# Kernel optimization log

Hardware: AMD Instinct MI355X
Metric: run time of the kernel (lower is better)

The kernel has to match this reference:

```python
import jax, jax.numpy as jnp
import numpy as np

D_MODEL = 1024
N_HEADS = 16
HEAD_DIM = D_MODEL // N_HEADS  # 64


def setup_inputs() -> dict:
    key = jax.random.key(0)
    k1, k2, k3 = jax.random.split(key, 3)
    x = jax.random.normal(k1, (2, 2048, D_MODEL), dtype=jnp.float32)
    # nn.Linear(d, 3d, bias=False): store transposed so y = x @ W
    w_qkv = jax.random.normal(k2, (D_MODEL, 3 * D_MODEL), dtype=jnp.float32) * (D_MODEL ** -0.5)
    w_proj = jax.random.normal(k3, (D_MODEL, D_MODEL), dtype=jnp.float32) * (D_MODEL ** -0.5)
    return {"x": x, "w_qkv": w_qkv, "w_proj": w_proj}


def reference(x, w_qkv, w_proj):
    b, n, _ = x.shape
    qkv = x @ w_qkv  # [b, n, 3*d_model]
    # einops 'b n (h d qkv) -> qkv b h n d': qkv axis is innermost of the split
    qkv = qkv.reshape(b, n, N_HEADS, HEAD_DIM, 3)
    q = jnp.moveaxis(qkv[..., 0], 1, 2)  # [b, h, n, d]
    k = jnp.moveaxis(qkv[..., 1], 1, 2)
    v = jnp.moveaxis(qkv[..., 2], 1, 2)
    scale = HEAD_DIM ** -0.5
    scores = jnp.einsum('bhqd,bhkd->bhqk', q, k) * scale  # [b, h, n, n]
    causal = jnp.tril(jnp.ones((n, n), dtype=bool))
    scores = jnp.where(causal[None, None], scores, -jnp.inf)
    attn = jax.nn.softmax(scores, axis=-1)
    out = jnp.einsum('bhqk,bhkd->bhqd', attn, v)  # [b, h, n, d]
    out = jnp.moveaxis(out, 1, 2).reshape(b, n, D_MODEL)  # 'b h n d -> b n (h d)'
    return out @ w_proj
```

## Files before the change

### kernel.cpp

```cpp
#include <hip/hip_runtime.h>
#include <cstdint>
#include <cstddef>

#define D_MODEL 1024
#define N_HEADS 16
#define HEAD_DIM 64
#define SEQ 2048
#define BATCH 2

typedef __attribute__((ext_vector_type(8))) short bf16x8;
typedef __attribute__((ext_vector_type(4))) float f32x4;

__device__ inline unsigned short f2bf(float f) {
    union { float f; unsigned u; } v; v.f = f;
    unsigned r = v.u + 0x7fffu + ((v.u >> 16) & 1u);
    return (unsigned short)(r >> 16);
}

__device__ __forceinline__ void gload_lds16(const unsigned short* g, unsigned short* l) {
    __builtin_amdgcn_global_load_lds(
        (const __attribute__((address_space(1))) unsigned int*)g,
        (__attribute__((address_space(3))) unsigned int*)l, 16, 0, 0);
}

__global__ __launch_bounds__(256) void convert_x_kernel(
    const float* __restrict__ X, unsigned short* __restrict__ Xb)
{
    const int idx = blockIdx.x * 256 + threadIdx.x;
    const float4* src = (const float4*)X;
    float4 v0 = src[idx * 2], v1 = src[idx * 2 + 1];
    union { unsigned short u[8]; uint4 v; } o;
    o.u[0] = f2bf(v0.x); o.u[1] = f2bf(v0.y); o.u[2] = f2bf(v0.z); o.u[3] = f2bf(v0.w);
    o.u[4] = f2bf(v1.x); o.u[5] = f2bf(v1.y); o.u[6] = f2bf(v1.z); o.u[7] = f2bf(v1.w);
    ((uint4*)Xb)[idx] = o.v;
}

__global__ __launch_bounds__(256) void convert_transpose_kernel(
    const float* __restrict__ W, unsigned short* __restrict__ Wt,
    int ncols, int nrows)
{
    __shared__ float t[32][33];
    const int c0 = blockIdx.x * 32, r0 = blockIdx.y * 32;
    const int a = threadIdx.x & 31, b = threadIdx.x >> 5;
#pragma unroll
    for (int i = 0; i < 32; i += 8)
        t[b + i][a] = W[(size_t)(r0 + b + i) * ncols + c0 + a];
    __syncthreads();
#pragma unroll
    for (int i = 0; i < 32; i += 8)
        Wt[(size_t)(c0 + b + i) * nrows + r0 + a] = f2bf(t[a][b + i]);
}

#define GEMM_MFMA_BODY(A_, B_, Kdim)                                           \
    const int tid = threadIdx.x;                                               \
    const int w = tid >> 6, lane = tid & 63;                                   \
    const int l15 = lane & 15, quad = lane >> 4;                               \
    const int wr = w >> 1, wc = w & 1;                                         \
    const int row0 = blockIdx.y * 128, col0 = blockIdx.x * 128;                \
    __shared__ unsigned short As[8192];                                        \
    __shared__ unsigned short Bs[8192];                                        \
    const f32x4 zero4 = {0.f, 0.f, 0.f, 0.f};                                  \
    f32x4 acc[4][4];                                                           \
    _Pragma("unroll") for (int i = 0; i < 4; i++)                              \
        _Pragma("unroll") for (int j = 0; j < 4; j++) acc[i][j] = zero4;       \
    for (int k0 = 0; k0 < (Kdim); k0 += 64) {                                  \
        __syncthreads();                                                       \
        _Pragma("unroll") for (int f = 0; f < 4; f++) {                        \
            const int fa = w * 4 + f;                                          \
            const int mt = fa >> 1, kt = fa & 1;                               \
            const int kcol = k0 + kt * 32 + quad * 8;                          \
            gload_lds16((A_) + (size_t)(row0 + mt * 16 + l15) * (Kdim) + kcol, \
                        &As[fa * 512 + lane * 8]);                             \
            gload_lds16((B_) + (size_t)(col0 + mt * 16 + l15) * (Kdim) + kcol, \
                        &Bs[fa * 512 + lane * 8]);                             \
        }                                                                      \
        __syncthreads();                                                       \
        _Pragma("unroll") for (int kt = 0; kt < 2; kt++) {                     \
            bf16x8 af[4], bf[4];                                               \
            _Pragma("unroll") for (int i = 0; i < 4; i++)                      \
                af[i] = *(const bf16x8*)&As[((wr * 4 + i) * 2 + kt) * 512 + lane * 8]; \
            _Pragma("unroll") for (int j = 0; j < 4; j++)                      \
                bf[j] = *(const bf16x8*)&Bs[((wc * 4 + j) * 2 + kt) * 512 + lane * 8]; \
            _Pragma("unroll") for (int i = 0; i < 4; i++)                      \
                _Pragma("unroll") for (int j = 0; j < 4; j++)                  \
                    acc[i][j] = __builtin_amdgcn_mfma_f32_16x16x32_bf16(       \
                        af[i], bf[j], acc[i][j], 0, 0, 0);                     \
        }                                                                      \
    }

__global__ __launch_bounds__(256) void gemm_qkv_mfma(
    const unsigned short* __restrict__ A, const unsigned short* __restrict__ B,
    unsigned short* __restrict__ Q, unsigned short* __restrict__ Kq,
    unsigned short* __restrict__ Vt)
{
    GEMM_MFMA_BODY(A, B, D_MODEL)
#pragma unroll
    for (int i = 0; i < 4; i++) {
#pragma unroll
        for (int r = 0; r < 4; r++) {
            const int row = row0 + wr * 64 + i * 16 + quad * 4 + r;
            const int bb = row >> 11, n = row & (SEQ - 1);
#pragma unroll
            for (int j = 0; j < 4; j++) {
                const int c = col0 + wc * 64 + j * 16 + l15;
                const int which = c % 3;
                const int dd = (c / 3) & (HEAD_DIM - 1);
                const int h = c / (3 * HEAD_DIM);
                const int bh = bb * N_HEADS + h;
                const unsigned short v = f2bf(acc[i][j][r]);
                if (which == 0)
                    Q[((size_t)bh * SEQ + n) * HEAD_DIM + dd] = v;
                else if (which == 1)
                    Kq[((size_t)bh * SEQ + n) * HEAD_DIM + dd] = v;
                else
                    Vt[((size_t)bh * HEAD_DIM + dd) * SEQ + n] = v;
            }
        }
    }
}

__global__ __launch_bounds__(256) void gemm_proj_mfma(
    const unsigned short* __restrict__ A, const unsigned short* __restrict__ B,
    float* __restrict__ C)
{
    GEMM_MFMA_BODY(A, B, D_MODEL)
#pragma unroll
    for (int i = 0; i < 4; i++) {
#pragma unroll
        for (int r = 0; r < 4; r++) {
            const int row = row0 + wr * 64 + i * 16 + quad * 4 + r;
#pragma unroll
            for (int j = 0; j < 4; j++) {
                const int c = col0 + wc * 64 + j * 16 + l15;
                C[(size_t)row * D_MODEL + c] = acc[i][j][r];
            }
        }
    }
}

#define PSTR 72

__global__ __launch_bounds__(256) void flash_attn_kernel(
    const unsigned short* __restrict__ Q,
    const unsigned short* __restrict__ K,
    const unsigned short* __restrict__ Vt,
    unsigned short* __restrict__ O)
{
    const int idx = blockIdx.x;
    const int bh = idx & 31;
    const int qt2 = idx >> 5;
    const int hi = qt2 >> 3, lo = qt2 & 7;
    const int qt = (hi == 0) ? lo : (hi == 1) ? 31 - lo : (hi == 2) ? lo + 8 : 23 - lo;

    const int tid = threadIdx.x;
    const int w = tid >> 6, lane = tid & 63;
    const int l15 = lane & 15, quad = lane >> 4;

    __shared__ unsigned short Ks[2][4096];
    __shared__ unsigned short Vs[2][4096];
    __shared__ unsigned short Ps[4][16 * PSTR];

    bf16x8 qf[2];
    {
        const unsigned short* qrow =
            Q + ((size_t)bh * SEQ + qt * 64 + w * 16 + l15) * HEAD_DIM;
        qf[0] = *(const bf16x8*)(qrow + quad * 8);
        qf[1] = *(const bf16x8*)(qrow + 32 + quad * 8);
    }

    const f32x4 zero4 = {0.f, 0.f, 0.f, 0.f};
    f32x4 o_acc[4] = {zero4, zero4, zero4, zero4};
    float m_i = -1e30f, l_i = 0.f;

    auto stage = [&](int bf, int kt_t) {
        const int key0 = kt_t * 64;
#pragma unroll
        for (int i = 0; i < 2; i++) {
            const int f = w * 2 + i;
            const int ct = f >> 1, kh = f & 1;
            gload_lds16(K + ((size_t)bh * SEQ + key0 + ct * 16 + l15) * HEAD_DIM
                          + kh * 32 + quad * 8,
                        &Ks[bf][f * 512 + lane * 8]);
            gload_lds16(Vt + ((size_t)bh * HEAD_DIM + ct * 16 + l15) * SEQ
                           + key0 + kh * 32 + quad * 8,
                        &Vs[bf][f * 512 + lane * 8]);
        }
    };

    stage(0, 0);
    int buf = 0;

    const int qg = qt * 64 + w * 16 + l15;

    for (int kt = 0; kt <= qt; kt++) {
        __syncthreads();
        if (kt < qt) stage(buf ^ 1, kt + 1);

        f32x4 st[4] = {zero4, zero4, zero4, zero4};
#pragma unroll
        for (int kh = 0; kh < 2; kh++) {
#pragma unroll
            for (int ct = 0; ct < 4; ct++) {
                bf16x8 kf = *(const bf16x8*)&Ks[buf][(ct * 2 + kh) * 512 + lane * 8];
                st[ct] = __builtin_amdgcn_mfma_f32_16x16x32_bf16(kf, qf[kh], st[ct], 0, 0, 0);
            }
        }

        const bool diag = (kt == qt);
        float mt = -1e30f;
#pragma unroll
        for (int ct = 0; ct < 4; ct++) {
#pragma unroll
            for (int r = 0; r < 4; r++) {
                float v = st[ct][r] * 0.125f;
                const int kg = kt * 64 + ct * 16 + quad * 4 + r;
                if (diag && kg > qg) v = -1e30f;
                st[ct][r] = v;
                mt = fmaxf(mt, v);
            }
        }
        mt = fmaxf(mt, __shfl_xor(mt, 16));
        mt = fmaxf(mt, __shfl_xor(mt, 32));

        const float mn = fmaxf(m_i, mt);
        const float alpha = __expf(m_i - mn);
        m_i = mn;

        float ls = 0.f;
#pragma unroll
        for (int ct = 0; ct < 4; ct++) {
            union { unsigned short u[4]; uint2 v; } pk;
#pragma unroll
            for (int r = 0; r < 4; r++) {
                float p = __expf(st[ct][r] - mn);
                ls += p;
                pk.u[r] = f2bf(p);
            }
            *(uint2*)&Ps[w][l15 * PSTR + ct * 16 + quad * 4] = pk.v;
        }
        ls += __shfl_xor(ls, 16);
        ls += __shfl_xor(ls, 32);
        l_i = l_i * alpha + ls;

        float ar[4];
#pragma unroll
        for (int r = 0; r < 4; r++)
            ar[r] = __shfl(alpha, (lane & 48) | (quad * 4 + r));
#pragma unroll
        for (int dt = 0; dt < 4; dt++)
#pragma unroll
            for (int r = 0; r < 4; r++)
                o_acc[dt][r] *= ar[r];

#pragma unroll
        for (int kh = 0; kh < 2; kh++) {
            bf16x8 pa = *(const bf16x8*)&Ps[w][l15 * PSTR + kh * 32 + quad * 8];
#pragma unroll
            for (int dt = 0; dt < 4; dt++) {
                bf16x8 vf = *(const bf16x8*)&Vs[buf][(dt * 2 + kh) * 512 + lane * 8];
                o_acc[dt] = __builtin_amdgcn_mfma_f32_16x16x32_bf16(pa, vf, o_acc[dt], 0, 0, 0);
            }
        }
        buf ^= 1;
    }

    const float linv = 1.0f / l_i;
    float lr[4];
#pragma unroll
    for (int r = 0; r < 4; r++)
        lr[r] = __shfl(linv, (lane & 48) | (quad * 4 + r));

    const int b = bh >> 4, h = bh & 15;
#pragma unroll
    for (int r = 0; r < 4; r++) {
        const int q = qt * 64 + w * 16 + quad * 4 + r;
        unsigned short* orow = O + ((size_t)b * SEQ + q) * D_MODEL + h * HEAD_DIM;
#pragma unroll
        for (int dt = 0; dt < 4; dt++)
            orow[dt * 16 + l15] = f2bf(o_acc[dt][r] * lr[r]);
    }
}

extern "C" void kernel_launch(void* const* d_in, const int* in_sizes, int n_in,
                              void* d_out, int out_size, void* d_ws, size_t ws_size,
                              hipStream_t stream) {
    const float* x      = (const float*)d_in[0];
    const float* w_qkv  = (const float*)d_in[1];
    const float* w_proj = (const float*)d_in[2];
    float* out = (float*)d_out;

    unsigned short* Xb  = (unsigned short*)d_ws;
    unsigned short* Wqt = Xb  + (size_t)4 * 1024 * 1024;
    unsigned short* Wpt = Wqt + (size_t)3 * 1024 * 1024;
    unsigned short* Qb  = Wpt + (size_t)1 * 1024 * 1024;
    unsigned short* Kb  = Qb  + (size_t)4 * 1024 * 1024;
    unsigned short* Vtb = Kb  + (size_t)4 * 1024 * 1024;
    unsigned short* Ob  = Vtb + (size_t)4 * 1024 * 1024;

    convert_x_kernel<<<dim3(2048), 256, 0, stream>>>(x, Xb);
    convert_transpose_kernel<<<dim3(3072 / 32, 1024 / 32), 256, 0, stream>>>(
        w_qkv, Wqt, 3 * D_MODEL, D_MODEL);
    convert_transpose_kernel<<<dim3(1024 / 32, 1024 / 32), 256, 0, stream>>>(
        w_proj, Wpt, D_MODEL, D_MODEL);

    gemm_qkv_mfma<<<dim3(3 * D_MODEL / 128, BATCH * SEQ / 128), 256, 0, stream>>>(
        Xb, Wqt, Qb, Kb, Vtb);

    flash_attn_kernel<<<dim3(SEQ / 64 * BATCH * N_HEADS), 256, 0, stream>>>(
        Qb, Kb, Vtb, Ob);

    gemm_proj_mfma<<<dim3(D_MODEL / 128, BATCH * SEQ / 128), 256, 0, stream>>>(
        Ob, Wpt, out);
}
```

Before: 244.6 us.

## Double-buffer LDS tiles in MFMA GEMM to overlap global loads with compute

Changes the shared GEMM body from a single 64-wide K tile with two barriers per step to two 32-wide LDS buffers with one barrier per step. Each step prefetches the next K slice into the other buffer, then runs MFMAs on the current one. The goal is to hide global-to-LDS load latency behind the matrix math. The trade-off is half as much work per barrier and twice as many loop iterations, and the overlap depends on how the compiler places vmcnt waits around the barrier.

```diff
diff --git a/kernel.cpp b/kernel.cpp
--- a/kernel.cpp
+++ b/kernel.cpp
@@ -57,35 +57,36 @@
     const int l15 = lane & 15, quad = lane >> 4;                               \
     const int wr = w >> 1, wc = w & 1;                                         \
     const int row0 = blockIdx.y * 128, col0 = blockIdx.x * 128;                \
-    __shared__ unsigned short As[8192];                                        \
-    __shared__ unsigned short Bs[8192];                                        \
+    __shared__ unsigned short As[2][4096];                                     \
+    __shared__ unsigned short Bs[2][4096];                                     \
     const f32x4 zero4 = {0.f, 0.f, 0.f, 0.f};                                  \
     f32x4 acc[4][4];                                                           \
     _Pragma("unroll") for (int i = 0; i < 4; i++)                              \
         _Pragma("unroll") for (int j = 0; j < 4; j++) acc[i][j] = zero4;       \
-    for (int k0 = 0; k0 < (Kdim); k0 += 64) {                                  \
+    auto stage_ = [&](int sb, int k0) {                                        \
+        _Pragma("unroll") for (int i = 0; i < 2; i++) {                        \
+            const int f = w * 2 + i;                                           \
+            gload_lds16((A_) + (size_t)(row0 + f * 16 + l15) * (Kdim) + k0 + quad * 8, \
+                        &As[sb][f * 512 + lane * 8]);                          \
+            gload_lds16((B_) + (size_t)(col0 + f * 16 + l15) * (Kdim) + k0 + quad * 8, \
+                        &Bs[sb][f * 512 + lane * 8]);                          \
+        }                                                                      \
+    };                                                                         \
+    stage_(0, 0);                                                              \
+    const int KITER = (Kdim) / 32;                                             \
+    for (int kt = 0; kt < KITER; kt++) {                                       \
+        const int sb = kt & 1;                                                 \
         __syncthreads();                                                       \
-        _Pragma("unroll") for (int f = 0; f < 4; f++) {                        \
-            const int fa = w * 4 + f;                                          \
-            const int mt = fa >> 1, kt = fa & 1;                               \
-            const int kcol = k0 + kt * 32 + quad * 8;                          \
-            gload_lds16((A_) + (size_t)(row0 + mt * 16 + l15) * (Kdim) + kcol, \
-                        &As[fa * 512 + lane * 8]);                             \
-            gload_lds16((B_) + (size_t)(col0 + mt * 16 + l15) * (Kdim) + kcol, \
-                        &Bs[fa * 512 + lane * 8]);                             \
-        }                                                                      \
-        __syncthreads();                                                       \
-        _Pragma("unroll") for (int kt = 0; kt < 2; kt++) {                     \
-            bf16x8 af[4], bf[4];                                               \
-            _Pragma("unroll") for (int i = 0; i < 4; i++)                      \
-                af[i] = *(const bf16x8*)&As[((wr * 4 + i) * 2 + kt) * 512 + lane * 8]; \
+        if (kt + 1 < KITER) stage_(sb ^ 1, (kt + 1) * 32);                     \
+        bf16x8 af[4], bfr[4];                                                  \
+        _Pragma("unroll") for (int i = 0; i < 4; i++)                          \
+            af[i] = *(const bf16x8*)&As[sb][(wr * 4 + i) * 512 + lane * 8];    \
+        _Pragma("unroll") for (int j = 0; j < 4; j++)                          \
+            bfr[j] = *(const bf16x8*)&Bs[sb][(wc * 4 + j) * 512 + lane * 8];   \
+        _Pragma("unroll") for (int i = 0; i < 4; i++)                          \
             _Pragma("unroll") for (int j = 0; j < 4; j++)                      \
-                bf[j] = *(const bf16x8*)&Bs[((wc * 4 + j) * 2 + kt) * 512 + lane * 8]; \
-            _Pragma("unroll") for (int i = 0; i < 4; i++)                      \
-                _Pragma("unroll") for (int j = 0; j < 4; j++)                  \
-                    acc[i][j] = __builtin_amdgcn_mfma_f32_16x16x32_bf16(       \
-                        af[i], bf[j], acc[i][j], 0, 0, 0);                     \
-        }                                                                      \
+                acc[i][j] = __builtin_amdgcn_mfma_f32_16x16x32_bf16(           \
+                    af[i], bfr[j], acc[i][j], 0, 0, 0);                        \
     }
 
 __global__ __launch_bounds__(256) void gemm_qkv_mfma(
```

New measurement: 231.9 us. 1.05x faster.

## Permute QKV weight columns, double-buffer GEMM LDS, transpose V separately

Applied to the files above, without the earlier changes.

The QKV weight transpose now permutes output columns so that Q, K and V each land in contiguous 1024-column blocks. This lets the QKV GEMM epilogue write each head's rows with coalesced stores instead of doing per-element mod-3 scatter and a strided V-transpose write. A separate v_transpose kernel then builds the transposed V layout that attention expects, through shared memory. The shared GEMM body also double-buffers its LDS tiles so the next k-tile loads while the current one is computed, at the cost of twice the shared memory, an extra kernel launch and an extra V buffer.

```diff
diff --git a/kernel.cpp b/kernel.cpp
--- a/kernel.cpp
+++ b/kernel.cpp
@@ -35,6 +35,24 @@
     ((uint4*)Xb)[idx] = o.v;
 }
 
+__global__ __launch_bounds__(256) void convert_transpose_qkv(
+    const float* __restrict__ W, unsigned short* __restrict__ Wt)
+{
+    __shared__ float t[32][33];
+    const int c0 = blockIdx.x * 32, r0 = blockIdx.y * 32;
+    const int a = threadIdx.x & 31, b = threadIdx.x >> 5;
+#pragma unroll
+    for (int i = 0; i < 32; i += 8)
+        t[b + i][a] = W[(size_t)(r0 + b + i) * (3 * D_MODEL) + c0 + a];
+    __syncthreads();
+#pragma unroll
+    for (int i = 0; i < 32; i += 8) {
+        const int c = c0 + b + i;
+        const int np = (c % 3) * 1024 + c / 3;
+        Wt[(size_t)np * D_MODEL + r0 + a] = f2bf(t[a][b + i]);
+    }
+}
+
 __global__ __launch_bounds__(256) void convert_transpose_kernel(
     const float* __restrict__ W, unsigned short* __restrict__ Wt,
     int ncols, int nrows)
@@ -49,6 +67,32 @@
 #pragma unroll
     for (int i = 0; i < 32; i += 8)
         Wt[(size_t)(c0 + b + i) * nrows + r0 + a] = f2bf(t[a][b + i]);
+}
+
+__global__ __launch_bounds__(256) void v_transpose(
+    const unsigned short* __restrict__ V, unsigned short* __restrict__ Vt)
+{
+    const int n0 = blockIdx.x * 64;
+    const int bh = blockIdx.y;
+    __shared__ unsigned short t[64 * 72];
+    const int tid = threadIdx.x;
+    const uint4* src = (const uint4*)(V + ((size_t)bh * SEQ + n0) * HEAD_DIM);
+#pragma unroll
+    for (int it = 0; it < 2; it++) {
+        const int lin = tid + it * 256;
+        const int row = lin >> 3, p = lin & 7;
+        ((uint4*)t)[row * 9 + p] = src[lin];
+    }
+    __syncthreads();
+#pragma unroll
+    for (int it = 0; it < 2; it++) {
+        const int lin = tid + it * 256;
+        const int drow = lin >> 3, p = lin & 7;
+        union { unsigned short u[8]; uint4 v; } o;
+#pragma unroll
+        for (int e = 0; e < 8; e++) o.u[e] = t[(p * 8 + e) * 72 + drow];
+        ((uint4*)(Vt + ((size_t)bh * HEAD_DIM + drow) * SEQ + n0))[p] = o.v;
+    }
 }
 
 #define GEMM_MFMA_BODY(A_, B_, Kdim)                                           \
@@ -57,43 +101,51 @@
     const int l15 = lane & 15, quad = lane >> 4;                               \
     const int wr = w >> 1, wc = w & 1;                                         \
     const int row0 = blockIdx.y * 128, col0 = blockIdx.x * 128;                \
-    __shared__ unsigned short As[8192];                                        \
-    __shared__ unsigned short Bs[8192];                                        \
+    __shared__ unsigned short As[2][8192];                                     \
+    __shared__ unsigned short Bs[2][8192];                                     \
     const f32x4 zero4 = {0.f, 0.f, 0.f, 0.f};                                  \
     f32x4 acc[4][4];                                                           \
     _Pragma("unroll") for (int i = 0; i < 4; i++)                              \
         _Pragma("unroll") for (int j = 0; j < 4; j++) acc[i][j] = zero4;       \
-    for (int k0 = 0; k0 < (Kdim); k0 += 64) {                                  \
+    auto stage_ = [&](int sb, int k0) {                                        \
+        _Pragma("unroll") for (int i = 0; i < 4; i++) {                        \
+            const int fa = w * 4 + i;                                          \
+            const int mt = fa >> 1, kh = fa & 1;                               \
+            const int kc = k0 + kh * 32 + quad * 8;                            \
+            gload_lds16((A_) + (size_t)(row0 + mt * 16 + l15) * (Kdim) + kc,   \
+                        &As[sb][fa * 512 + lane * 8]);                         \
+            gload_lds16((B_) + (size_t)(col0 + mt * 16 + l15) * (Kdim) + kc,   \
+                        &Bs[sb][fa * 512 + lane * 8]);                         \
+        }                                                                      \
+    };                                                                         \
+    stage_(0, 0);                                                              \
+    const int KITER = (Kdim) / 64;                                             \
+    for (int kt = 0; kt < KITER; kt++) {                                       \
+        const int sb = kt & 1;                                                 \
         __syncthreads();                                                       \
-        _Pragma("unroll") for (int f = 0; f < 4; f++) {                        \
-            const int fa = w * 4 + f;                                          \
-            const int mt = fa >> 1, kt = fa & 1;                               \
-            const int kcol = k0 + kt * 32 + quad * 8;                          \
-            gload_lds16((A_) + (size_t)(row0 + mt * 16 + l15) * (Kdim) + kcol, \
-                        &As[fa * 512 + lane * 8]);                             \
-            gload_lds16((B_) + (size_t)(col0 + mt * 16 + l15) * (Kdim) + kcol, \
-                        &Bs[fa * 512 + lane * 8]);                             \
-        }                                                                      \
-        __syncthreads();                                                       \
-        _Pragma("unroll") for (int kt = 0; kt < 2; kt++) {                     \
-            bf16x8 af[4], bf[4];                                               \
+        if (kt + 1 < KITER) stage_(sb ^ 1, (kt + 1) * 64);                     \
+        _Pragma("unroll") for (int kh = 0; kh < 2; kh++) {                     \
+            bf16x8 af[4], bfr[4];                                              \
             _Pragma("unroll") for (int i = 0; i < 4; i++)                      \
-                af[i] = *(const bf16x8*)&As[((wr * 4 + i) * 2 + kt) * 512 + lane * 8]; \
+                af[i] = *(const bf16x8*)&As[sb][((wr * 4 + i) * 2 + kh) * 512 + lane * 8]; \
             _Pragma("unroll") for (int j = 0; j < 4; j++)                      \
-                bf[j] = *(const bf16x8*)&Bs[((wc * 4 + j) * 2 + kt) * 512 + lane * 8]; \
+                bfr[j] = *(const bf16x8*)&Bs[sb][((wc * 4 + j) * 2 + kh) * 512 + lane * 8]; \
             _Pragma("unroll") for (int i = 0; i < 4; i++)                      \
                 _Pragma("unroll") for (int j = 0; j < 4; j++)                  \
                     acc[i][j] = __builtin_amdgcn_mfma_f32_16x16x32_bf16(       \
-                        af[i], bf[j], acc[i][j], 0, 0, 0);                     \
+                        af[i], bfr[j], acc[i][j], 0, 0, 0);                    \
         }                                                                      \
     }
 
 __global__ __launch_bounds__(256) void gemm_qkv_mfma(
     const unsigned short* __restrict__ A, const unsigned short* __restrict__ B,
     unsigned short* __restrict__ Q, unsigned short* __restrict__ Kq,
-    unsigned short* __restrict__ Vt)
+    unsigned short* __restrict__ Vb)
 {
     GEMM_MFMA_BODY(A, B, D_MODEL)
+    const int nbase = col0 + wc * 64;
+    const int which = nbase >> 10;
+    unsigned short* const dst = (which == 0) ? Q : (which == 1) ? Kq : Vb;
 #pragma unroll
     for (int i = 0; i < 4; i++) {
 #pragma unroll
@@ -102,18 +154,10 @@
             const int bb = row >> 11, n = row & (SEQ - 1);
 #pragma unroll
             for (int j = 0; j < 4; j++) {
-                const int c = col0 + wc * 64 + j * 16 + l15;
-                const int which = c % 3;
-                const int dd = (c / 3) & (HEAD_DIM - 1);
-                const int h = c / (3 * HEAD_DIM);
-                const int bh = bb * N_HEADS + h;
-                const unsigned short v = f2bf(acc[i][j][r]);
-                if (which == 0)
-                    Q[((size_t)bh * SEQ + n) * HEAD_DIM + dd] = v;
-                else if (which == 1)
-                    Kq[((size_t)bh * SEQ + n) * HEAD_DIM + dd] = v;
-                else
-                    Vt[((size_t)bh * HEAD_DIM + dd) * SEQ + n] = v;
+                const int idx = (nbase + j * 16 + l15) & 1023;
+                const int h = idx >> 6, dd = idx & 63;
+                dst[(((size_t)(bb * N_HEADS + h)) * SEQ + n) * HEAD_DIM + dd] =
+                    f2bf(acc[i][j][r]);
             }
         }
     }
@@ -294,17 +338,19 @@
     unsigned short* Wpt = Wqt + (size_t)3 * 1024 * 1024;
     unsigned short* Qb  = Wpt + (size_t)1 * 1024 * 1024;
     unsigned short* Kb  = Qb  + (size_t)4 * 1024 * 1024;
-    unsigned short* Vtb = Kb  + (size_t)4 * 1024 * 1024;
+    unsigned short* Vb  = Kb  + (size_t)4 * 1024 * 1024;
+    unsigned short* Vtb = Vb  + (size_t)4 * 1024 * 1024;
     unsigned short* Ob  = Vtb + (size_t)4 * 1024 * 1024;
 
     convert_x_kernel<<<dim3(2048), 256, 0, stream>>>(x, Xb);
-    convert_transpose_kernel<<<dim3(3072 / 32, 1024 / 32), 256, 0, stream>>>(
-        w_qkv, Wqt, 3 * D_MODEL, D_MODEL);
+    convert_transpose_qkv<<<dim3(3072 / 32, 1024 / 32), 256, 0, stream>>>(w_qkv, Wqt);
     convert_transpose_kernel<<<dim3(1024 / 32, 1024 / 32), 256, 0, stream>>>(
         w_proj, Wpt, D_MODEL, D_MODEL);
 
     gemm_qkv_mfma<<<dim3(3 * D_MODEL / 128, BATCH * SEQ / 128), 256, 0, stream>>>(
-        Xb, Wqt, Qb, Kb, Vtb);
+        Xb, Wqt, Qb, Kb, Vb);
+
+    v_transpose<<<dim3(SEQ / 64, BATCH * N_HEADS), 256, 0, stream>>>(Vb, Vtb);
 
     flash_attn_kernel<<<dim3(SEQ / 64 * BATCH * N_HEADS), 256, 0, stream>>>(
         Qb, Kb, Vtb, Ob);
```

After: 229.4 us. 6.2% less time.
